# Optimization experiments

Measured on AMD Instinct MI355X. Metric: run time of the kernel, lower is better.

## Reference

```python
import jax, jax.numpy as jnp
import numpy as np

D_MODEL = 512
NUM_HEADS = 8
HEAD_DIM = D_MODEL // NUM_HEADS
SEQ_LEN = 4096
BATCH = 2
D_FF = 4 * D_MODEL
EPS = 1e-5


def _layer_norm(x, g, b):
    mu = jnp.mean(x, axis=-1, keepdims=True)
    var = jnp.var(x, axis=-1, keepdims=True)
    return (x - mu) * jax.lax.rsqrt(var + EPS) * g + b


def setup_inputs() -> dict:
    key = jax.random.key(0)
    ks = jax.random.split(key, 12)
    s = 0.02
    inp = {
        "x": jax.random.normal(ks[0], (BATCH, SEQ_LEN, D_MODEL), jnp.float32),
        # Linear weights stored as [in, out] (y = x @ W + b)
        "Wq": jax.random.normal(ks[1], (D_MODEL, D_MODEL), jnp.float32) * s,
        "bq": jnp.zeros((D_MODEL,), jnp.float32),
        "Wk": jax.random.normal(ks[2], (D_MODEL, D_MODEL), jnp.float32) * s,
        "bk": jnp.zeros((D_MODEL,), jnp.float32),
        "Wv": jax.random.normal(ks[3], (D_MODEL, D_MODEL), jnp.float32) * s,
        "bv": jnp.zeros((D_MODEL,), jnp.float32),
        "Wo": jax.random.normal(ks[4], (D_MODEL, D_MODEL), jnp.float32) * s,
        "bo": jnp.zeros((D_MODEL,), jnp.float32),
        "ln1_g": jnp.ones((D_MODEL,), jnp.float32),
        "ln1_b": jnp.zeros((D_MODEL,), jnp.float32),
        "ln2_g": jnp.ones((D_MODEL,), jnp.float32),
        "ln2_b": jnp.zeros((D_MODEL,), jnp.float32),
        "W1": jax.random.normal(ks[5], (D_MODEL, D_FF), jnp.float32) * s,
        "b1": jnp.zeros((D_FF,), jnp.float32),
        "W2": jax.random.normal(ks[6], (D_FF, D_MODEL), jnp.float32) * s,
        "b2": jnp.zeros((D_MODEL,), jnp.float32),
    }
    return inp


def reference(x, Wq, bq, Wk, bk, Wv, bv, Wo, bo, ln1_g, ln1_b, ln2_g, ln2_b, W1, b1, W2, b2):
    B, S, D = x.shape
    residual = x
    h = _layer_norm(x, ln1_g, ln1_b)
    # project and split heads: [B, H, S, Dh]
    def split_heads(t):
        return t.reshape(B, S, NUM_HEADS, HEAD_DIM).transpose(0, 2, 1, 3)
    q = split_heads(h @ Wq + bq)
    k = split_heads(h @ Wk + bk)
    v = split_heads(h @ Wv + bv)
    scores = jnp.einsum("bhqd,bhkd->bhqk", q, k) / (HEAD_DIM ** 0.5)
    attn = jax.nn.softmax(scores, axis=-1)
    out = jnp.einsum("bhqk,bhkd->bhqd", attn, v)
    out = out.transpose(0, 2, 1, 3).reshape(B, S, D)
    out = out @ Wo + bo
    x1 = residual + out
    h2 = _layer_norm(x1, ln2_g, ln2_b)
    ff = jax.nn.gelu(h2 @ W1 + b1, approximate=False) @ W2 + b2
    return x1 + ff
```

## Files before the change

kernel.cpp:

```cpp
#include <hip/hip_runtime.h>
#include <hip/hip_bf16.h>
#include <math.h>

typedef __hip_bfloat16 bf16;

#define D_MODEL 512
#define NUM_HEADS 8
#define HEAD_DIM 64
#define SEQ_LEN 4096
#define BATCH 2
#define D_FF 2048
#define TOKENS (BATCH * SEQ_LEN)
#define QKV_STRIDE 1536
#define KSPLIT 3

typedef short short4v __attribute__((ext_vector_type(4)));
typedef short short8v __attribute__((ext_vector_type(8)));
typedef float float4v __attribute__((ext_vector_type(4)));

union frag_u { short8v v8; short4v v4[2]; short s[8]; };
union pack_u { unsigned u[2]; short4v v4; };

__device__ __forceinline__ float b2f(bf16 v) { return __bfloat162float(v); }
__device__ __forceinline__ bf16 f2b(float v) { return __float2bfloat16(v); }
__device__ __forceinline__ short f2bs(float v) { bf16 t = __float2bfloat16(v); return *(short*)&t; }

__device__ __forceinline__ unsigned pack_bf16(float lo, float hi) {
    unsigned a = __float_as_uint(hi) + 0x8000u;
    unsigned b = __float_as_uint(lo) + 0x8000u;
    return __builtin_amdgcn_perm(a, b, 0x07060302u);
}

#define AS1(p) ((__attribute__((address_space(1))) void*)(p))
#define AS3(p) ((__attribute__((address_space(3))) void*)(p))

__global__ void detect_kernel(const unsigned int* __restrict__ x, int* __restrict__ flag) {
    __shared__ int cnt;
    if (threadIdx.x == 0) cnt = 0;
    __syncthreads();
    unsigned int w = x[threadIdx.x];
    unsigned int e = (w >> 7) & 0xFFu;
    if (e >= 110 && e <= 140) atomicAdd(&cnt, 1);
    __syncthreads();
    if (threadIdx.x == 0) flag[0] = (cnt >= (int)(blockDim.x / 2)) ? 0 : 1;
}

__device__ __forceinline__ void do_tr(const void* __restrict__ src, bf16* __restrict__ dst,
                                      int K, int N, int n0, int k0, int fl, int tid,
                                      bf16 (*tile)[65]) {
    int c = tid & 63, r4 = tid >> 6;
#pragma unroll
    for (int t = 0; t < 16; t++) {
        int r = t * 4 + r4;
        size_t si = (size_t)(k0 + r) * N + n0 + c;
        float v = fl ? ((const float*)src)[si] : b2f(((const bf16*)src)[si]);
        tile[r][c] = f2b(v);
    }
    __syncthreads();
#pragma unroll
    for (int t = 0; t < 16; t++) {
        int r = t * 4 + r4;
        dst[(size_t)(n0 + r) * K + k0 + c] = tile[c][r];
    }
}

__global__ void prep_kernel(const void* Wq, const void* Wk, const void* Wv, const void* Wo,
                            const void* W1, const void* W2,
                            const void* bq, const void* bk, const void* bv, const void* bo,
                            const void* b1, const void* b2,
                            const void* g1, const void* e1, const void* g2, const void* e2,
                            bf16* __restrict__ Wqkvt ,
                            bf16* __restrict__ W1t, bf16* __restrict__ W2t,
                            bf16* __restrict__ small, const int* __restrict__ flag) {
    __shared__ bf16 tile[64][65];
    int blk = blockIdx.x, tid = threadIdx.x;
    int fl = *flag;
    if (blk < 256) {
        int z = blk >> 6, tt = blk & 63;
        const void* src = (z == 0) ? Wq : (z == 1) ? Wk : (z == 2) ? Wv : Wo;
        do_tr(src, Wqkvt + (size_t)z * 512 * 512, 512, 512, (tt & 7) * 64, (tt >> 3) * 64,
              fl, tid, tile);
    } else if (blk < 512) {
        int tt = blk - 256;
        do_tr(W1, W1t, 512, 2048, (tt & 31) * 64, (tt >> 5) * 64, fl, tid, tile);
    } else if (blk < 768) {
        int tt = blk - 512;
        do_tr(W2, W2t, 2048, 512, (tt & 7) * 64, (tt >> 3) * 64, fl, tid, tile);
    } else {
        int i = (blk - 768) * 256 + tid;
        const void* src; int off;
        if (i < 512)       { src = bq; off = 0; }
        else if (i < 1024) { src = bk; off = 512; }
        else if (i < 1536) { src = bv; off = 1024; }
        else if (i < 2048) { src = bo; off = 1536; }
        else if (i < 4096) { src = b1; off = 2048; }
        else if (i < 4608) { src = b2; off = 4096; }
        else if (i < 5120) { src = g1; off = 4608; }
        else if (i < 5632) { src = e1; off = 5120; }
        else if (i < 6144) { src = g2; off = 5632; }
        else               { src = e2; off = 6144; }
        int j = i - off;
        small[i] = fl ? f2b(((const float*)src)[j]) : ((const bf16*)src)[j];
    }
}

template <int MODE>
__global__ void ln_kernel(const void* __restrict__ xv, const bf16* __restrict__ g,
                          const bf16* __restrict__ b, bf16* __restrict__ out,
                          const int* __restrict__ flag) {
    int t = blockIdx.x;
    int tid = threadIdx.x;
    int fl = (MODE == 2) ? *flag : 0;
    float v0, v1;
    if (fl) {
        const float* xr = (const float*)xv + (size_t)t * D_MODEL;
        v0 = xr[tid]; v1 = xr[tid + 256];
    } else {
        const bf16* xr = (const bf16*)xv + (size_t)t * D_MODEL;
        v0 = b2f(xr[tid]); v1 = b2f(xr[tid + 256]);
    }
    float s = v0 + v1, ss = v0 * v0 + v1 * v1;
    for (int o = 32; o > 0; o >>= 1) {
        s += __shfl_down(s, o);
        ss += __shfl_down(ss, o);
    }
    __shared__ float rs[4], rss[4], stat[2];
    int w = tid >> 6, l = tid & 63;
    if (l == 0) { rs[w] = s; rss[w] = ss; }
    __syncthreads();
    if (tid == 0) {
        float S = rs[0] + rs[1] + rs[2] + rs[3];
        float SS = rss[0] + rss[1] + rss[2] + rss[3];
        float mu = S / (float)D_MODEL;
        float var = SS / (float)D_MODEL - mu * mu;
        stat[0] = mu;
        stat[1] = rsqrtf(var + 1e-5f);
    }
    __syncthreads();
    float mu = stat[0], rstd = stat[1];
    bf16* orow = out + (size_t)t * D_MODEL;
    orow[tid]       = f2b((v0 - mu) * rstd * b2f(g[tid])       + b2f(b[tid]));
    orow[tid + 256] = f2b((v1 - mu) * rstd * b2f(g[tid + 256]) + b2f(b[tid + 256]));
}

__device__ __forceinline__ float gelu_tanh(float v) {
    float u = 0.7978845608f * (v + 0.044715f * v * v * v);
    float e2 = __expf(-2.f * u);
    return v / (1.f + e2);
}

template <int ACT>
__global__ __launch_bounds__(256) void mfma_gemm(
    const bf16* __restrict__ A, const bf16* __restrict__ Wt,
    const bf16* __restrict__ bias, bf16* __restrict__ Cout,
    int M, int N, int K) {
    __shared__ bf16 As[128 * 64];
    __shared__ bf16 Bs[128 * 64];
    int tid = threadIdx.x, wave = tid >> 6, lane = tid & 63;
    int m = lane & 15, g = lane >> 4;
    int row0 = blockIdx.y * 128, col0 = blockIdx.x * 128;
    int R0 = (wave >> 1) * 64, C0 = (wave & 1) * 64;
    float4v acc[4][4] = {};

    int srow = lane >> 3;
    int scol = (lane & 7) * 8;
    const bf16* Ab = A  + (size_t)(row0 + wave * 8 + srow) * K + scol;
    const bf16* Bb = Wt + (size_t)(col0 + wave * 8 + srow) * K + scol;

    for (int k0 = 0; k0 < K; k0 += 64) {
#pragma unroll
        for (int t = 0; t < 4; t++) {
            int rbase = t * 32 + wave * 8;
            __builtin_amdgcn_global_load_lds(AS1(Ab + (size_t)(t * 32) * K + k0),
                                             AS3(&As[rbase * 64]), 16, 0, 0);
            __builtin_amdgcn_global_load_lds(AS1(Bb + (size_t)(t * 32) * K + k0),
                                             AS3(&Bs[rbase * 64]), 16, 0, 0);
        }
        __syncthreads();
#pragma unroll
        for (int kk = 0; kk < 2; kk++) {
            short8v fa[4], fb[4];
#pragma unroll
            for (int i = 0; i < 4; i++)
                fa[i] = *(const short8v*)&As[(R0 + i * 16 + m) * 64 + kk * 32 + g * 8];
#pragma unroll
            for (int j = 0; j < 4; j++)
                fb[j] = *(const short8v*)&Bs[(C0 + j * 16 + m) * 64 + kk * 32 + g * 8];
#pragma unroll
            for (int i = 0; i < 4; i++)
#pragma unroll
                for (int j = 0; j < 4; j++)
                    acc[i][j] = __builtin_amdgcn_mfma_f32_16x16x32_bf16(fa[i], fb[j], acc[i][j], 0, 0, 0);
        }
        __syncthreads();
    }

#pragma unroll
    for (int i = 0; i < 4; i++) {
#pragma unroll
        for (int r = 0; r < 4; r++) {
            int row = row0 + R0 + i * 16 + g * 4 + r;
#pragma unroll
            for (int j = 0; j < 4; j++) {
                int col = col0 + C0 + j * 16 + m;
                float v = acc[i][j][r] + b2f(bias[col]);
                if (ACT == 1) v = gelu_tanh(v);
                Cout[(size_t)row * N + col] = f2b(v);
            }
        }
    }
}

template <int RES, int OUTMODE>
__global__ __launch_bounds__(256) void mfma_gemm64(
    const bf16* __restrict__ A, const bf16* __restrict__ Wt,
    const bf16* __restrict__ bias, const void* __restrict__ res,
    void* __restrict__ Cout, const int* __restrict__ flag, int M, int N, int K) {
    __shared__ bf16 As[128 * 64];
    __shared__ bf16 Bs[64 * 64];
    int tid = threadIdx.x, wave = tid >> 6, lane = tid & 63;
    int m = lane & 15, g = lane >> 4;
    int row0 = blockIdx.y * 128, col0 = blockIdx.x * 64;
    int R0 = wave * 32;
    int fl = (OUTMODE == 2 || RES == 3) ? *flag : 0;
    float4v acc[2][4] = {};

    int srow = lane >> 3;
    int scol = (lane & 7) * 8;
    const bf16* Ab = A  + (size_t)(row0 + wave * 8 + srow) * K + scol;
    const bf16* Bb = Wt + (size_t)(col0 + wave * 8 + srow) * K + scol;

    for (int k0 = 0; k0 < K; k0 += 64) {
#pragma unroll
        for (int t = 0; t < 4; t++) {
            __builtin_amdgcn_global_load_lds(AS1(Ab + (size_t)(t * 32) * K + k0),
                                             AS3(&As[(t * 32 + wave * 8) * 64]), 16, 0, 0);
            if (t < 2)
                __builtin_amdgcn_global_load_lds(AS1(Bb + (size_t)(t * 32) * K + k0),
                                                 AS3(&Bs[(t * 32 + wave * 8) * 64]), 16, 0, 0);
        }
        __syncthreads();
#pragma unroll
        for (int kk = 0; kk < 2; kk++) {
            short8v fa[2], fb[4];
#pragma unroll
            for (int i = 0; i < 2; i++)
                fa[i] = *(const short8v*)&As[(R0 + i * 16 + m) * 64 + kk * 32 + g * 8];
#pragma unroll
            for (int j = 0; j < 4; j++)
                fb[j] = *(const short8v*)&Bs[(j * 16 + m) * 64 + kk * 32 + g * 8];
#pragma unroll
            for (int i = 0; i < 2; i++)
#pragma unroll
                for (int j = 0; j < 4; j++)
                    acc[i][j] = __builtin_amdgcn_mfma_f32_16x16x32_bf16(fa[i], fb[j], acc[i][j], 0, 0, 0);
        }
        __syncthreads();
    }

#pragma unroll
    for (int i = 0; i < 2; i++) {
#pragma unroll
        for (int r = 0; r < 4; r++) {
            int row = row0 + R0 + i * 16 + g * 4 + r;
#pragma unroll
            for (int j = 0; j < 4; j++) {
                int col = col0 + j * 16 + m;
                float v = acc[i][j][r] + b2f(bias[col]);
                size_t idx = (size_t)row * N + col;
                if (RES == 2) v += b2f(((const bf16*)res)[idx]);
                if (RES == 3) v += fl ? ((const float*)res)[idx]
                                      : b2f(((const bf16*)res)[idx]);
                if (OUTMODE == 0) ((bf16*)Cout)[idx] = f2b(v);
                else {
                    if (fl) ((float*)Cout)[idx] = v;
                    else ((bf16*)Cout)[idx] = f2b(v);
                }
            }
        }
    }
}

__global__ void v_transpose(const bf16* __restrict__ qkv, bf16* __restrict__ Vt_g) {
    __shared__ bf16 tile[64][65];
    int s0 = blockIdx.x * 64;
    int bh = blockIdx.y;
    int b = bh >> 3, h = bh & 7;
    int c = threadIdx.x & 63, r4 = threadIdx.x >> 6;
    const bf16* src = qkv + ((size_t)b * SEQ_LEN + s0) * QKV_STRIDE + 1024 + h * 64;
#pragma unroll
    for (int t = 0; t < 16; t++) {
        int r = t * 4 + r4;
        tile[r][c] = src[(size_t)r * QKV_STRIDE + c];
    }
    __syncthreads();
    bf16* dst = Vt_g + (size_t)bh * 64 * SEQ_LEN + s0;
#pragma unroll
    for (int t = 0; t < 16; t++) {
        int r = t * 4 + r4;
        dst[(size_t)r * SEQ_LEN + c] = tile[c][r];
    }
}

__global__ __launch_bounds__(256) void flash_attn(const bf16* __restrict__ Q,
                                                  const bf16* __restrict__ K,
                                                  const bf16* __restrict__ Vt_g,
                                                  bf16* __restrict__ Op,
                                                  float2* __restrict__ mlout) {
    __shared__ bf16 Ks[64][72];
    __shared__ bf16 Vt[64][68];
    __shared__ bf16 Pt[4][16][72];

    int tid = threadIdx.x;
    int wave = tid >> 6, lane = tid & 63;
    int m = lane & 15, g = lane >> 4;

    int bh = blockIdx.y;
    size_t base = (size_t)(bh >> 3) * SEQ_LEN * QKV_STRIDE + (size_t)(bh & 7) * HEAD_DIM;
    int q0w = blockIdx.x * 64 + wave * 16;

    short8v aQ[2];
    {
        const bf16* qp = Q + base + (size_t)(q0w + m) * QKV_STRIDE + g * 8;
#pragma unroll
        for (int c = 0; c < 2; c++) {
            frag_u u;
#pragma unroll
            for (int j = 0; j < 8; j++) u.s[j] = f2bs(b2f(qp[c * 32 + j]) * 0.125f);
            aQ[c] = u.v8;
        }
    }

    float mrow = -1e30f, lrow = 0.f;
    float4v oacc[4] = {};

    int sk = tid >> 2;
    int sd = (tid & 3) * 16;
    int vrow = tid >> 2;
    int vcol = (tid & 3) * 16;

    const unsigned short* Ku = (const unsigned short*)(K + base);
    const unsigned short* Vg = (const unsigned short*)Vt_g +
                               (size_t)bh * 64 * SEQ_LEN + (size_t)vrow * SEQ_LEN;

    int t0 = (blockIdx.z * 64) / KSPLIT;
    int t1 = ((blockIdx.z + 1) * 64) / KSPLIT;
    for (int t = t0; t < t1; t++) {
        int kt0 = t * 64;
        __syncthreads();
        {
            const unsigned short* kp = Ku + (size_t)(kt0 + sk) * QKV_STRIDE + sd;
            *(short8v*)&Ks[sk][sd]     = *(const short8v*)(kp);
            *(short8v*)&Ks[sk][sd + 8] = *(const short8v*)(kp + 8);
        }
        {
            frag_u u0, u1;
            u0.v8 = *(const short8v*)(Vg + kt0 + vcol);
            u1.v8 = *(const short8v*)(Vg + kt0 + vcol + 8);
            *(short4v*)&Vt[vrow][vcol]      = u0.v4[0];
            *(short4v*)&Vt[vrow][vcol + 4]  = u0.v4[1];
            *(short4v*)&Vt[vrow][vcol + 8]  = u1.v4[0];
            *(short4v*)&Vt[vrow][vcol + 12] = u1.v4[1];
        }
        __syncthreads();

        float4v st[4];
#pragma unroll
        for (int kt = 0; kt < 4; kt++) {
            short8v bK0 = *(const short8v*)&Ks[kt * 16 + m][g * 8];
            short8v bK1 = *(const short8v*)&Ks[kt * 16 + m][32 + g * 8];
            float4v a = {0.f, 0.f, 0.f, 0.f};
            a = __builtin_amdgcn_mfma_f32_16x16x32_bf16(bK0, aQ[0], a, 0, 0, 0);
            a = __builtin_amdgcn_mfma_f32_16x16x32_bf16(bK1, aQ[1], a, 0, 0, 0);
            st[kt] = a;
        }

        float tm = st[0][0];
#pragma unroll
        for (int kt = 0; kt < 4; kt++)
#pragma unroll
            for (int r = 0; r < 4; r++) tm = fmaxf(tm, st[kt][r]);
        tm = fmaxf(tm, __shfl_xor(tm, 16));
        tm = fmaxf(tm, __shfl_xor(tm, 32));
        float mnew = fmaxf(mrow, tm);
        float alpha = __expf(mrow - mnew);
        mrow = mnew;

        float psum = 0.f;
#pragma unroll
        for (int kt = 0; kt < 4; kt++) {
            float p0 = __expf(st[kt][0] - mnew);
            float p1 = __expf(st[kt][1] - mnew);
            float p2 = __expf(st[kt][2] - mnew);
            float p3 = __expf(st[kt][3] - mnew);
            psum += (p0 + p1) + (p2 + p3);
            pack_u pp;
            pp.u[0] = pack_bf16(p0, p1);
            pp.u[1] = pack_bf16(p2, p3);
            *(short4v*)&Pt[wave][m][kt * 16 + g * 4] = pp.v4;
        }
        lrow = lrow * alpha + psum;
#pragma unroll
        for (int dt = 0; dt < 4; dt++)
#pragma unroll
            for (int r = 0; r < 4; r++) oacc[dt][r] *= alpha;

        short8v bP[2];
#pragma unroll
        for (int c = 0; c < 2; c++)
            bP[c] = *(const short8v*)&Pt[wave][m][c * 32 + g * 8];

#pragma unroll
        for (int dt = 0; dt < 4; dt++) {
#pragma unroll
            for (int c = 0; c < 2; c++) {
                frag_u u;
                u.v4[0] = *(const short4v*)&Vt[dt * 16 + m][c * 32 + g * 8];
                u.v4[1] = *(const short4v*)&Vt[dt * 16 + m][c * 32 + g * 8 + 4];
                oacc[dt] = __builtin_amdgcn_mfma_f32_16x16x32_bf16(u.v8, bP[c], oacc[dt], 0, 0, 0);
            }
        }
    }

    lrow += __shfl_xor(lrow, 16);
    lrow += __shfl_xor(lrow, 32);

    size_t zoff = (size_t)blockIdx.z * NUM_HEADS * BATCH + bh;
    size_t pbase = zoff * (SEQ_LEN * (size_t)HEAD_DIM);
    int q = q0w + m;
    bf16* orow = Op + pbase + (size_t)q * HEAD_DIM;
#pragma unroll
    for (int dt = 0; dt < 4; dt++) {
        pack_u oo;
        oo.u[0] = pack_bf16(oacc[dt][0], oacc[dt][1]);
        oo.u[1] = pack_bf16(oacc[dt][2], oacc[dt][3]);
        *(short4v*)&orow[dt * 16 + g * 4] = oo.v4;
    }
    if (g == 0) mlout[zoff * SEQ_LEN + q] = make_float2(mrow, lrow);
}

__global__ void attn_merge(const bf16* __restrict__ Op, const float2* __restrict__ ml,
                           bf16* __restrict__ O) {
    int i = blockIdx.x * 256 + threadIdx.x;
    int d = i & 63;
    int q = (i >> 6) & (SEQ_LEN - 1);
    int bh = i >> 18;
    const int HQ = NUM_HEADS * BATCH * SEQ_LEN;
    float2 a0 = ml[bh * SEQ_LEN + q];
    float2 a1 = ml[HQ + bh * SEQ_LEN + q];
    float2 a2 = ml[2 * HQ + bh * SEQ_LEN + q];
    float M = fmaxf(a0.x, fmaxf(a1.x, a2.x));
    float w0 = __expf(a0.x - M), w1 = __expf(a1.x - M), w2 = __expf(a2.x - M);
    float inv = 1.f / (a0.y * w0 + a1.y * w1 + a2.y * w2);
    const size_t NP = (size_t)HQ * HEAD_DIM;
    float o = (b2f(Op[i]) * w0 + b2f(Op[NP + i]) * w1 + b2f(Op[2 * NP + i]) * w2) * inv;
    O[((size_t)((bh >> 3) * SEQ_LEN + q)) * D_MODEL + (bh & 7) * HEAD_DIM + d] = f2b(o);
}

extern "C" void kernel_launch(void* const* d_in, const int* in_sizes, int n_in,
                              void* d_out, int out_size, void* d_ws, size_t ws_size,
                              hipStream_t stream) {
    const void* x     = d_in[0];
    const void* Wq    = d_in[1];
    const void* bq    = d_in[2];
    const void* Wk    = d_in[3];
    const void* bk    = d_in[4];
    const void* Wv    = d_in[5];
    const void* bv    = d_in[6];
    const void* Wo    = d_in[7];
    const void* bo    = d_in[8];
    const void* ln1_g = d_in[9];
    const void* ln1_b = d_in[10];
    const void* ln2_g = d_in[11];
    const void* ln2_b = d_in[12];
    const void* W1    = d_in[13];
    const void* b1    = d_in[14];
    const void* W2    = d_in[15];
    const void* b2    = d_in[16];

    char* p = (char*)d_ws;
    int* flag = (int*)p;                      p += 256;
    size_t tok_d = (size_t)TOKENS * D_MODEL;
    char* region2 = p;                        p += (size_t)KSPLIT * NUM_HEADS * BATCH * SEQ_LEN * HEAD_DIM * 2;
    bf16* x1b   = (bf16*)region2;
    bf16* hb    = (bf16*)(region2 + tok_d * 2);
    bf16* Opart = (bf16*)region2;
    bf16*  bigA = (bf16*)p;                   p += (size_t)TOKENS * D_FF * 2;
    bf16*  qkvb = bigA;
    bf16*  ab   = bigA + (size_t)TOKENS * QKV_STRIDE;
    bf16*  ffb  = bigA;
    bf16*  Wqkvt = (bf16*)p;                  p += (size_t)QKV_STRIDE * D_MODEL * 2;
    bf16*  Wot   = (bf16*)p;                  p += (size_t)D_MODEL * D_MODEL * 2;
    bf16*  W1t   = (bf16*)p;                  p += (size_t)D_FF * D_MODEL * 2;
    bf16*  W2t   = (bf16*)p;                  p += (size_t)D_MODEL * D_FF * 2;
    bf16*  Vtg   = (bf16*)p;                  p += (size_t)NUM_HEADS * BATCH * HEAD_DIM * SEQ_LEN * 2;
    float2* mlb  = (float2*)p;                p += (size_t)KSPLIT * NUM_HEADS * BATCH * SEQ_LEN * sizeof(float2);
    bf16*  small = (bf16*)p;                  p += 6656 * 2;
    bf16* bias_qkv = small + 0;
    bf16* bias_o   = small + 1536;
    bf16* b1b      = small + 2048;
    bf16* b2b      = small + 4096;
    bf16* g1b      = small + 4608;
    bf16* be1b     = small + 5120;
    bf16* g2b      = small + 5632;
    bf16* be2b     = small + 6144;

    detect_kernel<<<1, 1024, 0, stream>>>((const unsigned int*)x, flag);

    prep_kernel<<<794, 256, 0, stream>>>(Wq, Wk, Wv, Wo, W1, W2,
                                         bq, bk, bv, bo, b1, b2,
                                         ln1_g, ln1_b, ln2_g, ln2_b,
                                         Wqkvt, W1t, W2t, small, flag);

    ln_kernel<2><<<TOKENS, 256, 0, stream>>>(x, g1b, be1b, hb, flag);

    mfma_gemm<0><<<dim3(QKV_STRIDE / 128, TOKENS / 128), 256, 0, stream>>>(
        hb, Wqkvt, bias_qkv, qkvb, TOKENS, QKV_STRIDE, D_MODEL);

    v_transpose<<<dim3(SEQ_LEN / 64, NUM_HEADS * BATCH), 256, 0, stream>>>(qkvb, Vtg);

    flash_attn<<<dim3(64, 16, KSPLIT), 256, 0, stream>>>(qkvb, qkvb + 512, Vtg,
                                                         Opart, mlb);
    attn_merge<<<(NUM_HEADS * BATCH * SEQ_LEN * HEAD_DIM) / 256, 256, 0, stream>>>(
        Opart, mlb, ab);

    mfma_gemm64<3, 0><<<dim3(D_MODEL / 64, TOKENS / 128), 256, 0, stream>>>(
        ab, Wot, bias_o, x, x1b, flag, TOKENS, D_MODEL, D_MODEL);

    ln_kernel<0><<<TOKENS, 256, 0, stream>>>(x1b, g2b, be2b, hb, flag);

    mfma_gemm<1><<<dim3(D_FF / 128, TOKENS / 128), 256, 0, stream>>>(
        hb, W1t, b1b, ffb, TOKENS, D_FF, D_MODEL);

    mfma_gemm64<2, 2><<<dim3(D_MODEL / 64, TOKENS / 128), 256, 0, stream>>>(
        ffb, W2t, b2b, x1b, d_out, flag, TOKENS, D_MODEL, D_FF);
}
```

Baseline: 404.2 us.

## Double per-wave query tile in flash attention, use exp2, fold detect into prep

Each wave in flash attention now processes 32 query rows instead of 16, so every K/V tile loaded into shared memory is reused by twice as many MFMAs. The KV split drops from 3 to 2, which halves the grid and simplifies the merge step. Softmax uses exp2 with log2e folded into the Q scale. The separate dtype-detect kernel is removed; prep_kernel computes the flag itself with a wave ballot, saving one launch. In exchange there is higher register pressure (launch bounds 256,4) and fewer blocks to fill the device.

```diff
diff --git a/kernel.cpp b/kernel.cpp
--- a/kernel.cpp
+++ b/kernel.cpp
@@ -12,7 +12,7 @@
 #define D_FF 2048
 #define TOKENS (BATCH * SEQ_LEN)
 #define QKV_STRIDE 1536
-#define KSPLIT 3
+#define KSPLIT 2
 
 typedef short short4v __attribute__((ext_vector_type(4)));
 typedef short short8v __attribute__((ext_vector_type(8)));
@@ -24,6 +24,7 @@
 __device__ __forceinline__ float b2f(bf16 v) { return __bfloat162float(v); }
 __device__ __forceinline__ bf16 f2b(float v) { return __float2bfloat16(v); }
 __device__ __forceinline__ short f2bs(float v) { bf16 t = __float2bfloat16(v); return *(short*)&t; }
+__device__ __forceinline__ float exp2fast(float x) { return __builtin_amdgcn_exp2f(x); }
 
 __device__ __forceinline__ unsigned pack_bf16(float lo, float hi) {
     unsigned a = __float_as_uint(hi) + 0x8000u;
@@ -34,15 +35,11 @@
 #define AS1(p) ((__attribute__((address_space(1))) void*)(p))
 #define AS3(p) ((__attribute__((address_space(3))) void*)(p))
 
-__global__ void detect_kernel(const unsigned int* __restrict__ x, int* __restrict__ flag) {
-    __shared__ int cnt;
-    if (threadIdx.x == 0) cnt = 0;
-    __syncthreads();
-    unsigned int w = x[threadIdx.x];
-    unsigned int e = (w >> 7) & 0xFFu;
-    if (e >= 110 && e <= 140) atomicAdd(&cnt, 1);
-    __syncthreads();
-    if (threadIdx.x == 0) flag[0] = (cnt >= (int)(blockDim.x / 2)) ? 0 : 1;
+__device__ __forceinline__ int self_detect(const unsigned* __restrict__ xw, int tid) {
+    unsigned w = xw[tid & 63];
+    unsigned e = (w >> 7) & 0xFFu;
+    unsigned long long b = __ballot(e >= 110 && e <= 140);
+    return __popcll(b) < 32;
 }
 
 __device__ __forceinline__ void do_tr(const void* __restrict__ src, bf16* __restrict__ dst,
@@ -64,17 +61,18 @@
     }
 }
 
-__global__ void prep_kernel(const void* Wq, const void* Wk, const void* Wv, const void* Wo,
-                            const void* W1, const void* W2,
+__global__ void prep_kernel(const void* x, const void* Wq, const void* Wk, const void* Wv,
+                            const void* Wo, const void* W1, const void* W2,
                             const void* bq, const void* bk, const void* bv, const void* bo,
                             const void* b1, const void* b2,
                             const void* g1, const void* e1, const void* g2, const void* e2,
                             bf16* __restrict__ Wqkvt ,
                             bf16* __restrict__ W1t, bf16* __restrict__ W2t,
-                            bf16* __restrict__ small, const int* __restrict__ flag) {
+                            bf16* __restrict__ small, int* __restrict__ flag) {
     __shared__ bf16 tile[64][65];
     int blk = blockIdx.x, tid = threadIdx.x;
-    int fl = *flag;
+    int fl = self_detect((const unsigned*)x, tid);
+    if (blk == 0 && tid == 0) flag[0] = fl;
     if (blk < 256) {
         int z = blk >> 6, tt = blk & 63;
         const void* src = (z == 0) ? Wq : (z == 1) ? Wk : (z == 2) ? Wv : Wo;
@@ -302,14 +300,14 @@
     }
 }
 
-__global__ __launch_bounds__(256) void flash_attn(const bf16* __restrict__ Q,
-                                                  const bf16* __restrict__ K,
-                                                  const bf16* __restrict__ Vt_g,
-                                                  bf16* __restrict__ Op,
-                                                  float2* __restrict__ mlout) {
+__global__ __launch_bounds__(256, 4) void flash_attn(const bf16* __restrict__ Q,
+                                                     const bf16* __restrict__ K,
+                                                     const bf16* __restrict__ Vt_g,
+                                                     bf16* __restrict__ Op,
+                                                     float2* __restrict__ mlout) {
     __shared__ bf16 Ks[64][72];
     __shared__ bf16 Vt[64][68];
-    __shared__ bf16 Pt[4][16][72];
+    __shared__ bf16 Pt[4][32][72];
 
     int tid = threadIdx.x;
     int wave = tid >> 6, lane = tid & 63;
@@ -317,34 +315,35 @@
 
     int bh = blockIdx.y;
     size_t base = (size_t)(bh >> 3) * SEQ_LEN * QKV_STRIDE + (size_t)(bh & 7) * HEAD_DIM;
-    int q0w = blockIdx.x * 64 + wave * 16;
-
-    short8v aQ[2];
-    {
-        const bf16* qp = Q + base + (size_t)(q0w + m) * QKV_STRIDE + g * 8;
+    int q0w = blockIdx.x * 128 + wave * 32;
+
+    const float qscale = 0.125f * 1.44269504f;
+    short8v aQ[2][2];
+#pragma unroll
+    for (int mt = 0; mt < 2; mt++) {
+        const bf16* qp = Q + base + (size_t)(q0w + mt * 16 + m) * QKV_STRIDE + g * 8;
 #pragma unroll
         for (int c = 0; c < 2; c++) {
             frag_u u;
 #pragma unroll
-            for (int j = 0; j < 8; j++) u.s[j] = f2bs(b2f(qp[c * 32 + j]) * 0.125f);
-            aQ[c] = u.v8;
-        }
-    }
-
-    float mrow = -1e30f, lrow = 0.f;
-    float4v oacc[4] = {};
-
-    int sk = tid >> 2;
-    int sd = (tid & 3) * 16;
-    int vrow = tid >> 2;
-    int vcol = (tid & 3) * 16;
+            for (int j = 0; j < 8; j++) u.s[j] = f2bs(b2f(qp[c * 32 + j]) * qscale);
+            aQ[mt][c] = u.v8;
+        }
+    }
+
+    float mrow[2] = {-1e30f, -1e30f};
+    float lrow[2] = {0.f, 0.f};
+    float4v oacc[2][4] = {};
+
+    int sk = tid >> 2, sd = (tid & 3) * 16;
+    int vrow = tid >> 2, vcol = (tid & 3) * 16;
 
     const unsigned short* Ku = (const unsigned short*)(K + base);
     const unsigned short* Vg = (const unsigned short*)Vt_g +
                                (size_t)bh * 64 * SEQ_LEN + (size_t)vrow * SEQ_LEN;
 
-    int t0 = (blockIdx.z * 64) / KSPLIT;
-    int t1 = ((blockIdx.z + 1) * 64) / KSPLIT;
+    int t0 = blockIdx.z * (64 / KSPLIT);
+    int t1 = t0 + 64 / KSPLIT;
     for (int t = t0; t < t1; t++) {
         int kt0 = t * 64;
         __syncthreads();
@@ -364,51 +363,59 @@
         }
         __syncthreads();
 
-        float4v st[4];
+        float4v st[2][4];
 #pragma unroll
         for (int kt = 0; kt < 4; kt++) {
             short8v bK0 = *(const short8v*)&Ks[kt * 16 + m][g * 8];
             short8v bK1 = *(const short8v*)&Ks[kt * 16 + m][32 + g * 8];
-            float4v a = {0.f, 0.f, 0.f, 0.f};
-            a = __builtin_amdgcn_mfma_f32_16x16x32_bf16(bK0, aQ[0], a, 0, 0, 0);
-            a = __builtin_amdgcn_mfma_f32_16x16x32_bf16(bK1, aQ[1], a, 0, 0, 0);
-            st[kt] = a;
-        }
-
-        float tm = st[0][0];
-#pragma unroll
-        for (int kt = 0; kt < 4; kt++)
-#pragma unroll
-            for (int r = 0; r < 4; r++) tm = fmaxf(tm, st[kt][r]);
-        tm = fmaxf(tm, __shfl_xor(tm, 16));
-        tm = fmaxf(tm, __shfl_xor(tm, 32));
-        float mnew = fmaxf(mrow, tm);
-        float alpha = __expf(mrow - mnew);
-        mrow = mnew;
-
-        float psum = 0.f;
-#pragma unroll
-        for (int kt = 0; kt < 4; kt++) {
-            float p0 = __expf(st[kt][0] - mnew);
-            float p1 = __expf(st[kt][1] - mnew);
-            float p2 = __expf(st[kt][2] - mnew);
-            float p3 = __expf(st[kt][3] - mnew);
-            psum += (p0 + p1) + (p2 + p3);
-            pack_u pp;
-            pp.u[0] = pack_bf16(p0, p1);
-            pp.u[1] = pack_bf16(p2, p3);
-            *(short4v*)&Pt[wave][m][kt * 16 + g * 4] = pp.v4;
-        }
-        lrow = lrow * alpha + psum;
-#pragma unroll
-        for (int dt = 0; dt < 4; dt++)
-#pragma unroll
-            for (int r = 0; r < 4; r++) oacc[dt][r] *= alpha;
-
-        short8v bP[2];
-#pragma unroll
-        for (int c = 0; c < 2; c++)
-            bP[c] = *(const short8v*)&Pt[wave][m][c * 32 + g * 8];
+#pragma unroll
+            for (int mt = 0; mt < 2; mt++) {
+                float4v a = {0.f, 0.f, 0.f, 0.f};
+                a = __builtin_amdgcn_mfma_f32_16x16x32_bf16(bK0, aQ[mt][0], a, 0, 0, 0);
+                a = __builtin_amdgcn_mfma_f32_16x16x32_bf16(bK1, aQ[mt][1], a, 0, 0, 0);
+                st[mt][kt] = a;
+            }
+        }
+
+#pragma unroll
+        for (int mt = 0; mt < 2; mt++) {
+            float tm = st[mt][0][0];
+#pragma unroll
+            for (int kt = 0; kt < 4; kt++)
+#pragma unroll
+                for (int r = 0; r < 4; r++) tm = fmaxf(tm, st[mt][kt][r]);
+            tm = fmaxf(tm, __shfl_xor(tm, 16));
+            tm = fmaxf(tm, __shfl_xor(tm, 32));
+            float mnew = fmaxf(mrow[mt], tm);
+            float alpha = exp2fast(mrow[mt] - mnew);
+            mrow[mt] = mnew;
+
+            float psum = 0.f;
+#pragma unroll
+            for (int kt = 0; kt < 4; kt++) {
+                float p0 = exp2fast(st[mt][kt][0] - mnew);
+                float p1 = exp2fast(st[mt][kt][1] - mnew);
+                float p2 = exp2fast(st[mt][kt][2] - mnew);
+                float p3 = exp2fast(st[mt][kt][3] - mnew);
+                psum += (p0 + p1) + (p2 + p3);
+                pack_u pp;
+                pp.u[0] = pack_bf16(p0, p1);
+                pp.u[1] = pack_bf16(p2, p3);
+                *(short4v*)&Pt[wave][mt * 16 + m][kt * 16 + g * 4] = pp.v4;
+            }
+            lrow[mt] = lrow[mt] * alpha + psum;
+#pragma unroll
+            for (int dt = 0; dt < 4; dt++)
+#pragma unroll
+                for (int r = 0; r < 4; r++) oacc[mt][dt][r] *= alpha;
+        }
+
+        short8v bP[2][2];
+#pragma unroll
+        for (int mt = 0; mt < 2; mt++)
+#pragma unroll
+            for (int c = 0; c < 2; c++)
+                bP[mt][c] = *(const short8v*)&Pt[wave][mt * 16 + m][c * 32 + g * 8];
 
 #pragma unroll
         for (int dt = 0; dt < 4; dt++) {
@@ -417,26 +424,31 @@
                 frag_u u;
                 u.v4[0] = *(const short4v*)&Vt[dt * 16 + m][c * 32 + g * 8];
                 u.v4[1] = *(const short4v*)&Vt[dt * 16 + m][c * 32 + g * 8 + 4];
-                oacc[dt] = __builtin_amdgcn_mfma_f32_16x16x32_bf16(u.v8, bP[c], oacc[dt], 0, 0, 0);
+#pragma unroll
+                for (int mt = 0; mt < 2; mt++)
+                    oacc[mt][dt] = __builtin_amdgcn_mfma_f32_16x16x32_bf16(u.v8, bP[mt][c], oacc[mt][dt], 0, 0, 0);
             }
         }
     }
-
-    lrow += __shfl_xor(lrow, 16);
-    lrow += __shfl_xor(lrow, 32);
 
     size_t zoff = (size_t)blockIdx.z * NUM_HEADS * BATCH + bh;
     size_t pbase = zoff * (SEQ_LEN * (size_t)HEAD_DIM);
-    int q = q0w + m;
-    bf16* orow = Op + pbase + (size_t)q * HEAD_DIM;
-#pragma unroll
-    for (int dt = 0; dt < 4; dt++) {
-        pack_u oo;
-        oo.u[0] = pack_bf16(oacc[dt][0], oacc[dt][1]);
-        oo.u[1] = pack_bf16(oacc[dt][2], oacc[dt][3]);
-        *(short4v*)&orow[dt * 16 + g * 4] = oo.v4;
-    }
-    if (g == 0) mlout[zoff * SEQ_LEN + q] = make_float2(mrow, lrow);
+#pragma unroll
+    for (int mt = 0; mt < 2; mt++) {
+        float l = lrow[mt];
+        l += __shfl_xor(l, 16);
+        l += __shfl_xor(l, 32);
+        int q = q0w + mt * 16 + m;
+        bf16* orow = Op + pbase + (size_t)q * HEAD_DIM;
+#pragma unroll
+        for (int dt = 0; dt < 4; dt++) {
+            pack_u oo;
+            oo.u[0] = pack_bf16(oacc[mt][dt][0], oacc[mt][dt][1]);
+            oo.u[1] = pack_bf16(oacc[mt][dt][2], oacc[mt][dt][3]);
+            *(short4v*)&orow[dt * 16 + g * 4] = oo.v4;
+        }
+        if (g == 0) mlout[zoff * SEQ_LEN + q] = make_float2(mrow[mt], l);
+    }
 }
 
 __global__ void attn_merge(const bf16* __restrict__ Op, const float2* __restrict__ ml,
@@ -448,12 +460,11 @@
     const int HQ = NUM_HEADS * BATCH * SEQ_LEN;
     float2 a0 = ml[bh * SEQ_LEN + q];
     float2 a1 = ml[HQ + bh * SEQ_LEN + q];
-    float2 a2 = ml[2 * HQ + bh * SEQ_LEN + q];
-    float M = fmaxf(a0.x, fmaxf(a1.x, a2.x));
-    float w0 = __expf(a0.x - M), w1 = __expf(a1.x - M), w2 = __expf(a2.x - M);
-    float inv = 1.f / (a0.y * w0 + a1.y * w1 + a2.y * w2);
+    float M = fmaxf(a0.x, a1.x);
+    float w0 = exp2fast(a0.x - M), w1 = exp2fast(a1.x - M);
+    float inv = 1.f / (a0.y * w0 + a1.y * w1);
     const size_t NP = (size_t)HQ * HEAD_DIM;
-    float o = (b2f(Op[i]) * w0 + b2f(Op[NP + i]) * w1 + b2f(Op[2 * NP + i]) * w2) * inv;
+    float o = (b2f(Op[i]) * w0 + b2f(Op[NP + i]) * w1) * inv;
     O[((size_t)((bh >> 3) * SEQ_LEN + q)) * D_MODEL + (bh & 7) * HEAD_DIM + d] = f2b(o);
 }
 
@@ -481,7 +492,7 @@
     char* p = (char*)d_ws;
     int* flag = (int*)p;                      p += 256;
     size_t tok_d = (size_t)TOKENS * D_MODEL;
-    char* region2 = p;                        p += (size_t)KSPLIT * NUM_HEADS * BATCH * SEQ_LEN * HEAD_DIM * 2;
+    char* region2 = p;                        p += 2 * tok_d * 2;
     bf16* x1b   = (bf16*)region2;
     bf16* hb    = (bf16*)(region2 + tok_d * 2);
     bf16* Opart = (bf16*)region2;
@@ -505,9 +516,7 @@
     bf16* g2b      = small + 5632;
     bf16* be2b     = small + 6144;
 
-    detect_kernel<<<1, 1024, 0, stream>>>((const unsigned int*)x, flag);
-
-    prep_kernel<<<794, 256, 0, stream>>>(Wq, Wk, Wv, Wo, W1, W2,
+    prep_kernel<<<794, 256, 0, stream>>>(x, Wq, Wk, Wv, Wo, W1, W2,
                                          bq, bk, bv, bo, b1, b2,
                                          ln1_g, ln1_b, ln2_g, ln2_b,
                                          Wqkvt, W1t, W2t, small, flag);
@@ -519,8 +528,8 @@
 
     v_transpose<<<dim3(SEQ_LEN / 64, NUM_HEADS * BATCH), 256, 0, stream>>>(qkvb, Vtg);
 
-    flash_attn<<<dim3(64, 16, KSPLIT), 256, 0, stream>>>(qkvb, qkvb + 512, Vtg,
-                                                         Opart, mlb);
+    flash_attn<<<dim3(SEQ_LEN / 128, 16, KSPLIT), 256, 0, stream>>>(
+        qkvb, qkvb + 512, Vtg, Opart, mlb);
     attn_merge<<<(NUM_HEADS * BATCH * SEQ_LEN * HEAD_DIM) / 256, 256, 0, stream>>>(
         Opart, mlb, ab);
 
```

Result: faster. 369.7 us (-8.5%).
